# Kernel tuning notes

Measured on AMD Instinct MI355X. Metric: run time of the kernel, lower is better.

Reference implementation:

```python
import jax, jax.numpy as jnp
import numpy as np

B, T, K, V, D, C = 16, 16, 4, 10003, 256, 64  # batch, traj_len, beam, lid_size+3, dim_embed_loc, dim_com


def setup_inputs() -> dict:
    key = jax.random.key(0)
    ks = jax.random.split(key, 9)
    return {
        "loc_tar": jax.random.randint(ks[0], (B, T), 0, V),
        "zs": jax.random.normal(ks[1], (B, D), jnp.float32),
        "zt": jax.random.normal(ks[2], (B, D), jnp.float32),
        "E": jax.random.normal(ks[3], (V, D), jnp.float32) * 0.02,    # loc embedding table
        "W_v": jax.random.normal(ks[4], (D, V), jnp.float32) * 0.02,  # decoder output proj
        "b_v": jnp.zeros((V,), jnp.float32),
        "W_c": jax.random.normal(ks[5], (D, C), jnp.float32) * 0.05,  # LocCompressor
        "b_c": jnp.zeros((C,), jnp.float32),
        "W_t": jax.random.normal(ks[6], (C,), jnp.float32) * 0.05,    # temporal decoder
        "W_zt": jax.random.normal(ks[7], (D,), jnp.float32) * 0.05,
    }


def _decode(loc_tar, zs, E, W_v, b_v):
    # Beam-search decode faithful to the torch inference branch:
    # per-step full-seq decoder fwd, log_softmax, topk, (log-prob) product,
    # descending sort over M*K candidates, gather top 2K chains.
    chain_r = loc_tar.at[:, 1:].set(0)   # [B,T]; keep BOS, zero rest
    zs_r = zs                            # [B,D]
    prob = None
    for i in range(T - 1):
        emb = E[chain_r]                                     # [N,T,D] gather
        h = emb + zs_r[:, None, :]
        logp = jax.nn.log_softmax(h @ W_v + b_v, axis=-1)    # [N,T,V]
        p_i, idx_i = jax.lax.top_k(logp[:, i, :], K)         # [N,K]
        if i == 0:
            chain_r = jnp.repeat(chain_r, K, axis=0).at[:, 1].set(idx_i.reshape(-1))  # [B*K,T]
            prob = p_i                                       # [B,K]
            zs_r = jnp.repeat(zs_r, K, axis=0)
        else:
            M = chain_r.shape[0] // B                        # K at i=1, 2K after
            # NOTE: original multiplies log-probs (faithful to source)
            prob2 = (prob[:, :, None] * p_i.reshape(B, M, K)).reshape(B, M * K)
            order = jnp.argsort(-prob2, axis=-1)             # descending sort
            prob = jnp.take_along_axis(prob2, order, axis=-1)[:, :2 * K]
            ch = jnp.repeat(chain_r, K, axis=0).at[:, i + 1].set(idx_i.reshape(-1))
            ch = ch.reshape(B, M * K, T)
            chain_r = ch[jnp.arange(B)[:, None], order[:, :2 * K]].reshape(-1, T)  # [B*2K,T]
            zs_r = jnp.repeat(zs, 2 * K, axis=0)
    return chain_r.reshape(B, -1, T)[:, 0, 1:-1]             # best beam, [B,T-2]


def reference(loc_tar, zs, zt, E, W_v, b_v, W_c, b_c, W_t, W_zt):
    loc_chain = _decode(loc_tar, zs, E, W_v, b_v)            # [B,T-2] int
    loc_info = jnp.tanh(E[loc_chain] @ W_c + b_c)            # LocCompressor, [B,T-2,C]
    tim_chain = loc_info @ W_t + (zt @ W_zt)[:, None]        # temporal decoder, [B,T-2]
    return loc_chain, tim_chain
```

## Files before the change

### kernel.cpp

```cpp
#include <hip/hip_runtime.h>
#include <math.h>

#define BB 16
#define TT 16
#define KK 4
#define VV 10003
#define DD 256
#define CC 64
#define RPB 4
#define VT  1280
#define NVT 8
#define VP 10016
#define FNEG (-1e30f)

typedef float f32x4 __attribute__((ext_vector_type(4)));
typedef float f32x4u __attribute__((ext_vector_type(4), aligned(4)));

struct L4 { float v0, v1, v2, v3; int i0, i1, i2, i3; };

__device__ __forceinline__ void l4_init(L4 &l) {
  l.v0 = l.v1 = l.v2 = l.v3 = FNEG;
  l.i0 = l.i1 = l.i2 = l.i3 = 0x7fffffff;
}
__device__ __forceinline__ bool better(float v, int ix, float v2, int ix2) {
  return (v > v2) || (v == v2 && ix < ix2);
}
__device__ __forceinline__ void l4_insert(L4 &l, float v, int ix) {
  const bool c0 = better(v, ix, l.v0, l.i0);
  const bool c1 = better(v, ix, l.v1, l.i1);
  const bool c2 = better(v, ix, l.v2, l.i2);
  const bool c3 = better(v, ix, l.v3, l.i3);
  l.v3 = c3 ? (c2 ? l.v2 : v) : l.v3;  l.i3 = c3 ? (c2 ? l.i2 : ix) : l.i3;
  l.v2 = c2 ? (c1 ? l.v1 : v) : l.v2;  l.i2 = c2 ? (c1 ? l.i1 : ix) : l.i2;
  l.v1 = c1 ? (c0 ? l.v0 : v) : l.v1;  l.i1 = c1 ? (c0 ? l.i0 : ix) : l.i1;
  l.v0 = c0 ? v : l.v0;                l.i0 = c0 ? ix : l.i0;
}
__device__ __forceinline__ void l4_merge(L4 &a, const L4 &b) {
  l4_insert(a, b.v0, b.i0);
  l4_insert(a, b.v1, b.i1);
  l4_insert(a, b.v2, b.i2);
  l4_insert(a, b.v3, b.i3);
}
__device__ __forceinline__ L4 l4_shfl_xor(const L4 &a, int off) {
  L4 o;
  o.v0 = __shfl_xor(a.v0, off); o.i0 = __shfl_xor(a.i0, off);
  o.v1 = __shfl_xor(a.v1, off); o.i1 = __shfl_xor(a.i1, off);
  o.v2 = __shfl_xor(a.v2, off); o.i2 = __shfl_xor(a.i2, off);
  o.v3 = __shfl_xor(a.v3, off); o.i3 = __shfl_xor(a.i3, off);
  return o;
}

__device__ float np_block_sum(const float* a, int n) {
  float r0=a[0],r1=a[1],r2=a[2],r3=a[3],r4=a[4],r5=a[5],r6=a[6],r7=a[7];
  int i;
  for (i = 8; i + 8 <= n; i += 8) {
    r0 += a[i+0]; r1 += a[i+1]; r2 += a[i+2]; r3 += a[i+3];
    r4 += a[i+4]; r5 += a[i+5]; r6 += a[i+6]; r7 += a[i+7];
  }
  float res = ((r0 + r1) + (r2 + r3)) + ((r4 + r5) + (r6 + r7));
  for (; i < n; ++i) res += a[i];
  return res;
}

__global__ void k_init(const int* __restrict__ loc_tar, int* __restrict__ chainA) {
  int t = threadIdx.x;
  int b = t >> 4, j = t & 15;
  chainA[t] = (j == 0) ? loc_tar[b * TT] : 0;
}

__global__ __launch_bounds__(256, 1)
void k_gemm(const float* __restrict__ E, const float* __restrict__ zs,
            const float* __restrict__ Wv, const float* __restrict__ bv,
            const int* __restrict__ chain, float* __restrict__ Lg,
            int step, int N, int Mshift) {
  __shared__ __align__(16) float xs[RPB * DD];
  __shared__ int cs[RPB];

  const int t = threadIdx.x;
  const int tile = blockIdx.x % NVT;
  const int n0 = (blockIdx.x / NVT) * RPB;
  const int v0 = tile * VT;

  const int v4 = v0 + (t << 2);
  const int v1 = v0 + 1024 + t;
  const int v1ok = (v1 < VV);
  const int v1c = v1ok ? v1 : (VV - 1);

  if (t < RPB) {
    int n = n0 + t;
    int c = chain[n * TT + step];
    if ((unsigned)c >= VV) c = 0;
    cs[t] = c;
  }
  __syncthreads();

  for (int e = t; e < RPB * DD; e += 256) {
    int r = e >> 8, d = e & 255;
    int n = n0 + r;
    int b = n >> Mshift;
    xs[e] = E[cs[r] * DD + d] + zs[b * DD + d];
  }
  __syncthreads();

  const float* w4p = Wv + v4;
  const float* w1p = Wv + v1c;

  float acc4[RPB][4];
  float acc1[RPB];
#pragma unroll
  for (int r = 0; r < RPB; ++r) {
    acc1[r] = 0.f;
#pragma unroll
    for (int j = 0; j < 4; ++j) acc4[r][j] = 0.f;
  }

  f32x4u w4A[8], w4B[8];
  float  w1A[8], w1B[8];
  f32x4  h0A[RPB], h1A[RPB], h0B[RPB], h1B[RPB];

#pragma unroll
  for (int u = 0; u < 8; ++u) {
    w4A[u] = *(const f32x4u*)(w4p + (size_t)u * VV);
    w1A[u] = w1p[(size_t)u * VV];
  }
#pragma unroll
  for (int r = 0; r < RPB; ++r) {
    h0A[r] = *(const f32x4*)(xs + r * DD);
    h1A[r] = *(const f32x4*)(xs + r * DD + 4);
  }

  for (int d0 = 0; d0 < DD; d0 += 16) {
    const int dB = d0 + 8;
#pragma unroll
    for (int u = 0; u < 8; ++u) {
      w4B[u] = *(const f32x4u*)(w4p + (size_t)(dB + u) * VV);
      w1B[u] = w1p[(size_t)(dB + u) * VV];
    }
#pragma unroll
    for (int r = 0; r < RPB; ++r) {
      h0B[r] = *(const f32x4*)(xs + r * DD + dB);
      h1B[r] = *(const f32x4*)(xs + r * DD + dB + 4);
    }

#pragma unroll
    for (int u = 0; u < 8; ++u) {
#pragma unroll
      for (int r = 0; r < RPB; ++r) {
        const float hv = (u < 4) ? h0A[r][u] : h1A[r][u - 4];
#pragma unroll
        for (int j = 0; j < 4; ++j) acc4[r][j] = fmaf(hv, w4A[u][j], acc4[r][j]);
        acc1[r] = fmaf(hv, w1A[u], acc1[r]);
      }
    }

    const int dA = (d0 + 16 < DD) ? (d0 + 16) : 0;
#pragma unroll
    for (int u = 0; u < 8; ++u) {
      w4A[u] = *(const f32x4u*)(w4p + (size_t)(dA + u) * VV);
      w1A[u] = w1p[(size_t)(dA + u) * VV];
    }
#pragma unroll
    for (int r = 0; r < RPB; ++r) {
      h0A[r] = *(const f32x4*)(xs + r * DD + dA);
      h1A[r] = *(const f32x4*)(xs + r * DD + dA + 4);
    }

#pragma unroll
    for (int u = 0; u < 8; ++u) {
#pragma unroll
      for (int r = 0; r < RPB; ++r) {
        const float hv = (u < 4) ? h0B[r][u] : h1B[r][u - 4];
#pragma unroll
        for (int j = 0; j < 4; ++j) acc4[r][j] = fmaf(hv, w4B[u][j], acc4[r][j]);
        acc1[r] = fmaf(hv, w1B[u], acc1[r]);
      }
    }
  }

  const f32x4u bv4 = *(const f32x4u*)(bv + v4);
#pragma unroll
  for (int r = 0; r < RPB; ++r) {
    f32x4 o;
#pragma unroll
    for (int j = 0; j < 4; ++j) o[j] = acc4[r][j] + bv4[j];
    *(f32x4*)(Lg + (size_t)(n0 + r) * VP + v4) = o;
  }
  if (v1ok) {
    const float bvv = bv[v1];
#pragma unroll
    for (int r = 0; r < RPB; ++r)
      Lg[(size_t)(n0 + r) * VP + v1] = acc1[r] + bvv;
  }
}

__global__ __launch_bounds__(1024)
void k_red(const float* __restrict__ Lg, float* __restrict__ topP,
           int* __restrict__ topI) {
  __shared__ __align__(16) float row[VV];
  __shared__ float wmax[16];
  __shared__ float wv4[16 * 4];
  __shared__ int   wi4[16 * 4];

  const int n = blockIdx.x;
  const int t = threadIdx.x;
  const int lane = t & 63;
  const int wid = t >> 6;
  const float* grow = Lg + (size_t)n * VP;

  const int va = t << 2;
  const int vb = 4096 + (t << 2);
  const int vc = 8192 + (t << 2);
  f32x4 xa = *(const f32x4*)(grow + va);
  f32x4 xb = *(const f32x4*)(grow + vb);
  f32x4 xc;
  const bool cfull = (vc + 3 < VV);
  if (cfull) {
    xc = *(const f32x4*)(grow + vc);
  } else {
#pragma unroll
    for (int j = 0; j < 4; ++j) xc[j] = (vc + j < VV) ? grow[vc + j] : FNEG;
  }

  float m = FNEG;
  L4 top; l4_init(top);
#pragma unroll
  for (int j = 0; j < 4; ++j) { float x = xa[j]; if (x > m) m = x; l4_insert(top, x, va + j); }
#pragma unroll
  for (int j = 0; j < 4; ++j) { float x = xb[j]; if (x > m) m = x; l4_insert(top, x, vb + j); }
#pragma unroll
  for (int j = 0; j < 4; ++j) {
    if (vc + j < VV) { float x = xc[j]; if (x > m) m = x; l4_insert(top, x, vc + j); }
  }

  for (int off = 32; off; off >>= 1) {
    float m2 = __shfl_xor(m, off);
    if (m2 > m) m = m2;
    L4 o = l4_shfl_xor(top, off);
    l4_merge(top, o);
  }
  if (lane == 0) {
    wmax[wid] = m;
    wv4[wid * 4 + 0] = top.v0; wi4[wid * 4 + 0] = top.i0;
    wv4[wid * 4 + 1] = top.v1; wi4[wid * 4 + 1] = top.i1;
    wv4[wid * 4 + 2] = top.v2; wi4[wid * 4 + 2] = top.i2;
    wv4[wid * 4 + 3] = top.v3; wi4[wid * 4 + 3] = top.i3;
  }
  __syncthreads();

  float mm = wmax[lane & 15];
#pragma unroll
  for (int off = 8; off; off >>= 1) {
    float m2 = __shfl_xor(mm, off);
    if (m2 > mm) mm = m2;
  }
  const float gm = mm;

  L4 aa; l4_init(aa);
  if (wid == 0) {
    const int g = lane & 15;
    aa.v0 = wv4[g * 4 + 0]; aa.i0 = wi4[g * 4 + 0];
    aa.v1 = wv4[g * 4 + 1]; aa.i1 = wi4[g * 4 + 1];
    aa.v2 = wv4[g * 4 + 2]; aa.i2 = wi4[g * 4 + 2];
    aa.v3 = wv4[g * 4 + 3]; aa.i3 = wi4[g * 4 + 3];
#pragma unroll
    for (int off = 8; off; off >>= 1) {
      L4 o = l4_shfl_xor(aa, off);
      l4_merge(aa, o);
    }
  }

  {
    f32x4 ea, eb;
#pragma unroll
    for (int j = 0; j < 4; ++j) ea[j] = (float)exp((double)(xa[j] - gm));
#pragma unroll
    for (int j = 0; j < 4; ++j) eb[j] = (float)exp((double)(xb[j] - gm));
    *(f32x4*)(row + va) = ea;
    *(f32x4*)(row + vb) = eb;
    if (cfull) {
      f32x4 ec;
#pragma unroll
      for (int j = 0; j < 4; ++j) ec[j] = (float)exp((double)(xc[j] - gm));
      *(f32x4*)(row + vc) = ec;
    } else {
#pragma unroll
      for (int j = 0; j < 4; ++j)
        if (vc + j < VV) row[vc + j] = (float)exp((double)(xc[j] - gm));
    }
  }
  __syncthreads();

  if (t < 64) {
    int base = 0, nn = VV;
#pragma unroll
    for (int k = 5; k >= 0; --k) {
      int half = nn >> 1;
      int n2 = half - (half & 7);
      if ((t >> k) & 1) { base += n2; nn -= n2; } else nn = n2;
    }
    int half = nn >> 1;
    int n2 = half - (half & 7);
    float sa = np_block_sum(&row[base], n2);
    float sb = np_block_sum(&row[base + n2], nn - n2);
    float v = sa + sb;
#pragma unroll
    for (int l = 0; l < 6; ++l) {
      float x0 = __shfl(v, t * 2);
      float x1 = __shfl(v, t * 2 + 1);
      v = x0 + x1;
    }
    if (t == 0) {
      float ls = (float)log((double)v);
      topP[n * 4 + 0] = (aa.v0 - gm) - ls;  topI[n * 4 + 0] = aa.i0;
      topP[n * 4 + 1] = (aa.v1 - gm) - ls;  topI[n * 4 + 1] = aa.i1;
      topP[n * 4 + 2] = (aa.v2 - gm) - ls;  topI[n * 4 + 2] = aa.i2;
      topP[n * 4 + 3] = (aa.v3 - gm) - ls;  topI[n * 4 + 3] = aa.i3;
    }
  }
}

__global__ __launch_bounds__(512)
void k_beam(const float* __restrict__ topP, const int* __restrict__ topI,
            float* __restrict__ prob, const int* __restrict__ chain_cur,
            int* __restrict__ chain_next, int step) {
  __shared__ int sel_src[BB][8];
  __shared__ int sel_tok[BB][8];

  const int tid = threadIdx.x;
  const int b = tid >> 5;
  const int c = tid & 31;

  if (step == 0) {
    for (int e = tid; e < BB * KK * TT; e += 512) {
      int dst = e >> 4, q = e & 15;
      int bb = dst >> 2, kk = dst & 3;
      int val;
      if (q == 1) {
        int tok = topI[bb * 4 + kk]; if ((unsigned)tok >= VV) tok = 0;
        val = tok;
      } else {
        val = chain_cur[bb * TT + q];
      }
      chain_next[dst * TT + q] = val;
    }
    if (tid < BB * KK) {
      int bb = tid >> 2, kk = tid & 3;
      prob[bb * 8 + kk] = topP[bb * 4 + kk];
    }
    return;
  }

  const int M = (step == 1) ? 4 : 8;
  const int nc = M * 4;

  float act;
  if (c < nc) {
    int m = c >> 2, k = c & 3;
    act = prob[b * 8 + m] * topP[(b * M + m) * 4 + k];
  } else {
    act = -INFINITY;
  }

  for (int j = 0; j < 8; ++j) {
    float rv = act; int ri = c;
#pragma unroll
    for (int off = 1; off < 32; off <<= 1) {
      float v2 = __shfl_xor(rv, off, 32);
      int   i2 = __shfl_xor(ri, off, 32);
      if (v2 > rv || (v2 == rv && i2 < ri)) { rv = v2; ri = i2; }
    }
    if (c == ri) act = -INFINITY;
    if (c == 0) {
      int m = ri >> 2, k = ri & 3;
      int src = b * M + m;
      int tok = topI[src * 4 + k]; if ((unsigned)tok >= VV) tok = 0;
      sel_src[b][j] = src;
      sel_tok[b][j] = tok;
      prob[b * 8 + j] = rv;
    }
  }
  __syncthreads();

  for (int e = tid; e < BB * 8 * TT; e += 512) {
    int dst = e >> 4, q = e & 15;
    int bb = dst >> 3, j = dst & 7;
    int src = sel_src[bb][j];
    int val = (q == step + 1) ? sel_tok[bb][j] : chain_cur[src * TT + q];
    chain_next[dst * TT + q] = val;
  }
}

__global__ __launch_bounds__(64)
void k_final(const int* __restrict__ chain, const float* __restrict__ E,
             const float* __restrict__ Wc, const float* __restrict__ bc,
             const float* __restrict__ Wt, const float* __restrict__ zt,
             const float* __restrict__ Wzt, float* __restrict__ out) {
  int blk = blockIdx.x;
  int b = blk / (TT - 2), t = blk % (TT - 2);
  int lane = threadIdx.x;
  int loc = chain[(b * 8) * TT + 1 + t];
  if ((unsigned)loc >= VV) loc = 0;
  double acc = (double)bc[lane];
  const float* er = E + loc * DD;
  for (int d = 0; d < DD; ++d) acc += (double)er[d] * (double)Wc[d * CC + lane];
  double val = tanh(acc) * (double)Wt[lane];
  const float* ztr = zt + b * DD;
#pragma unroll
  for (int q = 0; q < 4; ++q) val += (double)ztr[lane * 4 + q] * (double)Wzt[lane * 4 + q];
  for (int off = 32; off; off >>= 1) val += __shfl_down(val, off);
  if (lane == 0) {
    out[b * (TT - 2) + t] = (float)loc;
    out[BB * (TT - 2) + b * (TT - 2) + t] = (float)val;
  }
}

extern "C" void kernel_launch(void* const* d_in, const int* in_sizes, int n_in,
                              void* d_out, int out_size, void* d_ws, size_t ws_size,
                              hipStream_t stream) {
  const int*   loc_tar = (const int*)  d_in[0];
  const float* zs      = (const float*)d_in[1];
  const float* zt      = (const float*)d_in[2];
  const float* E       = (const float*)d_in[3];
  const float* Wv      = (const float*)d_in[4];
  const float* bv      = (const float*)d_in[5];
  const float* Wc      = (const float*)d_in[6];
  const float* bc      = (const float*)d_in[7];
  const float* Wt      = (const float*)d_in[8];
  const float* Wzt     = (const float*)d_in[9];
  float* out = (float*)d_out;

  char* w = (char*)d_ws;
  float* Lg     = (float*)(w);
  float* topP   = (float*)(w + 5128192);
  int*   topI   = (int*)  (w + 5130240);
  float* prob   = (float*)(w + 5132288);
  int*   chainA = (int*)  (w + 5132800);
  int*   chainB = (int*)  (w + 5140992);

  k_init<<<1, 256, 0, stream>>>(loc_tar, chainA);

  int N = BB;
  int* cur = chainA;
  int* nxt = chainB;
  for (int i = 0; i < TT - 1; ++i) {
    int Mshift = (i == 0) ? 0 : ((i == 1) ? 2 : 3);
    int nrg = N / RPB;
    k_gemm<<<nrg * NVT, 256, 0, stream>>>(E, zs, Wv, bv, cur, Lg, i, N, Mshift);
    k_red<<<N, 1024, 0, stream>>>(Lg, topP, topI);
    k_beam<<<1, 512, 0, stream>>>(topP, topI, prob, cur, nxt, i);
    int* t2 = cur; cur = nxt; nxt = t2;
    N = (i == 0) ? BB * KK : BB * 2 * KK;
  }

  k_final<<<BB * (TT - 2), 64, 0, stream>>>(cur, E, Wc, bc, Wt, zt, Wzt, out);
}
```

Before: 1.017 ms.

## Fold beam selection into GEMM prologue and parallelize softmax sum

Drops the separate k_init and k_beam launches. Each k_gemm block now recomputes the beam top-2K selection redundantly in its prologue to get its input tokens, and block 0 writes the updated chain and prob buffers, which are double-buffered. k_final does the last selection itself. The softmax denominator in k_red now uses all 1024 threads (128 leaves, 8 lanes each, shuffle-reduced) instead of 64 serial leaves. This saves launch gaps and the serial sum, at the cost of redundant per-block selection work and a changed summation order.

```diff
diff --git a/kernel.cpp b/kernel.cpp
--- a/kernel.cpp
+++ b/kernel.cpp
@@ -50,31 +50,19 @@
   return o;
 }
 
-__device__ float np_block_sum(const float* a, int n) {
-  float r0=a[0],r1=a[1],r2=a[2],r3=a[3],r4=a[4],r5=a[5],r6=a[6],r7=a[7];
-  int i;
-  for (i = 8; i + 8 <= n; i += 8) {
-    r0 += a[i+0]; r1 += a[i+1]; r2 += a[i+2]; r3 += a[i+3];
-    r4 += a[i+4]; r5 += a[i+5]; r6 += a[i+6]; r7 += a[i+7];
-  }
-  float res = ((r0 + r1) + (r2 + r3)) + ((r4 + r5) + (r6 + r7));
-  for (; i < n; ++i) res += a[i];
-  return res;
-}
-
-__global__ void k_init(const int* __restrict__ loc_tar, int* __restrict__ chainA) {
-  int t = threadIdx.x;
-  int b = t >> 4, j = t & 15;
-  chainA[t] = (j == 0) ? loc_tar[b * TT] : 0;
-}
-
 __global__ __launch_bounds__(256, 1)
 void k_gemm(const float* __restrict__ E, const float* __restrict__ zs,
             const float* __restrict__ Wv, const float* __restrict__ bv,
-            const int* __restrict__ chain, float* __restrict__ Lg,
-            int step, int N, int Mshift) {
+            const int* __restrict__ loc_tar,
+            const float* __restrict__ topP, const int* __restrict__ topI,
+            const float* __restrict__ probIn, const int* __restrict__ chainIn,
+            float* __restrict__ probOut, int* __restrict__ chainOut,
+            float* __restrict__ Lg, int step, int N, int Mshift) {
   __shared__ __align__(16) float xs[RPB * DD];
   __shared__ int cs[RPB];
+  __shared__ int selSrc[BB][8];
+  __shared__ int selTok[BB][8];
+  __shared__ float prS[BB * 8];
 
   const int t = threadIdx.x;
   const int tile = blockIdx.x % NVT;
@@ -86,13 +74,79 @@
   const int v1ok = (v1 < VV);
   const int v1c = v1ok ? v1 : (VV - 1);
 
+  if (step >= 2) {
+    const int M = (step == 2) ? 4 : 8;
+    const int nc = M * 4;
+    const int c = t & 31;
+    const int bh = t >> 5;
+    for (int h = 0; h < 2; ++h) {
+      const int b = bh + h * 8;
+      float act;
+      if (c < nc) {
+        int mi = c >> 2, k = c & 3;
+        act = probIn[b * 8 + mi] * topP[(b * M + mi) * 4 + k];
+      } else {
+        act = -INFINITY;
+      }
+      for (int j = 0; j < 8; ++j) {
+        float rv = act; int ri = c;
+#pragma unroll
+        for (int off = 1; off < 32; off <<= 1) {
+          float v2 = __shfl_xor(rv, off, 32);
+          int   i2 = __shfl_xor(ri, off, 32);
+          if (v2 > rv || (v2 == rv && i2 < ri)) { rv = v2; ri = i2; }
+        }
+        if (c == ri) act = -INFINITY;
+        if (c == 0) {
+          int mi = ri >> 2, k = ri & 3;
+          int src = b * M + mi;
+          int tok = topI[src * 4 + k]; if ((unsigned)tok >= VV) tok = 0;
+          selSrc[b][j] = src;
+          selTok[b][j] = tok;
+          prS[b * 8 + j] = rv;
+        }
+      }
+    }
+    __syncthreads();
+  }
+
   if (t < RPB) {
     int n = n0 + t;
-    int c = chain[n * TT + step];
-    if ((unsigned)c >= VV) c = 0;
-    cs[t] = c;
+    int ctok;
+    if (step == 0)      ctok = loc_tar[n * TT];
+    else if (step == 1) ctok = topI[(n >> 2) * 4 + (n & 3)];
+    else                ctok = selTok[n >> 3][n & 7];
+    if ((unsigned)ctok >= VV) ctok = 0;
+    cs[t] = ctok;
   }
   __syncthreads();
+
+  if (blockIdx.x == 0 && step >= 1) {
+    if (step == 1) {
+      for (int e = t; e < BB * KK * TT; e += 256) {
+        int dst = e >> 4, q = e & 15;
+        int bb = dst >> 2, kk = dst & 3;
+        int val;
+        if (q == 1) { int tok = topI[bb * 4 + kk]; if ((unsigned)tok >= VV) tok = 0; val = tok; }
+        else if (q == 0) val = loc_tar[bb * TT];
+        else val = 0;
+        chainOut[dst * TT + q] = val;
+      }
+      if (t < BB * KK) {
+        int bb = t >> 2, kk = t & 3;
+        probOut[bb * 8 + kk] = topP[bb * 4 + kk];
+      }
+    } else {
+      for (int e = t; e < BB * 8 * TT; e += 256) {
+        int dst = e >> 4, q = e & 15;
+        int bb = dst >> 3, j = dst & 7;
+        int src = selSrc[bb][j];
+        int val = (q == step) ? selTok[bb][j] : chainIn[src * TT + q];
+        chainOut[dst * TT + q] = val;
+      }
+      if (t < BB * 8) probOut[t] = prS[t];
+    }
+  }
 
   for (int e = t; e < RPB * DD; e += 256) {
     int r = e >> 8, d = e & 255;
@@ -200,6 +254,7 @@
   __shared__ float wmax[16];
   __shared__ float wv4[16 * 4];
   __shared__ int   wi4[16 * 4];
+  __shared__ float leafS[128];
 
   const int n = blockIdx.x;
   const int t = threadIdx.x;
@@ -290,19 +345,31 @@
   }
   __syncthreads();
 
-  if (t < 64) {
+  {
+    const int g = t >> 3, j = t & 7;
     int base = 0, nn = VV;
 #pragma unroll
-    for (int k = 5; k >= 0; --k) {
+    for (int k = 6; k >= 0; --k) {
       int half = nn >> 1;
       int n2 = half - (half & 7);
-      if ((t >> k) & 1) { base += n2; nn -= n2; } else nn = n2;
-    }
-    int half = nn >> 1;
-    int n2 = half - (half & 7);
-    float sa = np_block_sum(&row[base], n2);
-    float sb = np_block_sum(&row[base + n2], nn - n2);
-    float v = sa + sb;
+      if ((g >> k) & 1) { base += n2; nn -= n2; } else nn = n2;
+    }
+    const float* a = row + base;
+    const int full = nn & ~7;
+    float r = a[j];
+    for (int i = 8 + j; i < full; i += 8) r += a[i];
+    float s = r + __shfl_xor(r, 1);
+    s = s + __shfl_xor(s, 2);
+    s = s + __shfl_xor(s, 4);
+    if (j == 0) {
+      for (int i = full; i < nn; ++i) s += a[i];
+      leafS[g] = s;
+    }
+  }
+  __syncthreads();
+
+  if (t < 64) {
+    float v = leafS[2 * t] + leafS[2 * t + 1];
 #pragma unroll
     for (int l = 0; l < 6; ++l) {
       float x0 = __shfl(v, t * 2);
@@ -319,87 +386,31 @@
   }
 }
 
-__global__ __launch_bounds__(512)
-void k_beam(const float* __restrict__ topP, const int* __restrict__ topI,
-            float* __restrict__ prob, const int* __restrict__ chain_cur,
-            int* __restrict__ chain_next, int step) {
-  __shared__ int sel_src[BB][8];
-  __shared__ int sel_tok[BB][8];
-
-  const int tid = threadIdx.x;
-  const int b = tid >> 5;
-  const int c = tid & 31;
-
-  if (step == 0) {
-    for (int e = tid; e < BB * KK * TT; e += 512) {
-      int dst = e >> 4, q = e & 15;
-      int bb = dst >> 2, kk = dst & 3;
-      int val;
-      if (q == 1) {
-        int tok = topI[bb * 4 + kk]; if ((unsigned)tok >= VV) tok = 0;
-        val = tok;
-      } else {
-        val = chain_cur[bb * TT + q];
-      }
-      chain_next[dst * TT + q] = val;
-    }
-    if (tid < BB * KK) {
-      int bb = tid >> 2, kk = tid & 3;
-      prob[bb * 8 + kk] = topP[bb * 4 + kk];
-    }
-    return;
-  }
-
-  const int M = (step == 1) ? 4 : 8;
-  const int nc = M * 4;
-
-  float act;
-  if (c < nc) {
-    int m = c >> 2, k = c & 3;
-    act = prob[b * 8 + m] * topP[(b * M + m) * 4 + k];
-  } else {
-    act = -INFINITY;
-  }
-
-  for (int j = 0; j < 8; ++j) {
-    float rv = act; int ri = c;
-#pragma unroll
-    for (int off = 1; off < 32; off <<= 1) {
-      float v2 = __shfl_xor(rv, off, 32);
-      int   i2 = __shfl_xor(ri, off, 32);
-      if (v2 > rv || (v2 == rv && i2 < ri)) { rv = v2; ri = i2; }
-    }
-    if (c == ri) act = -INFINITY;
-    if (c == 0) {
-      int m = ri >> 2, k = ri & 3;
-      int src = b * M + m;
-      int tok = topI[src * 4 + k]; if ((unsigned)tok >= VV) tok = 0;
-      sel_src[b][j] = src;
-      sel_tok[b][j] = tok;
-      prob[b * 8 + j] = rv;
-    }
-  }
-  __syncthreads();
-
-  for (int e = tid; e < BB * 8 * TT; e += 512) {
-    int dst = e >> 4, q = e & 15;
-    int bb = dst >> 3, j = dst & 7;
-    int src = sel_src[bb][j];
-    int val = (q == step + 1) ? sel_tok[bb][j] : chain_cur[src * TT + q];
-    chain_next[dst * TT + q] = val;
-  }
-}
-
 __global__ __launch_bounds__(64)
-void k_final(const int* __restrict__ chain, const float* __restrict__ E,
+void k_final(const int* __restrict__ chainIn, const float* __restrict__ probIn,
+             const float* __restrict__ topP, const int* __restrict__ topI,
+             const float* __restrict__ E,
              const float* __restrict__ Wc, const float* __restrict__ bc,
              const float* __restrict__ Wt, const float* __restrict__ zt,
              const float* __restrict__ Wzt, float* __restrict__ out) {
   int blk = blockIdx.x;
-  int b = blk / (TT - 2), t = blk % (TT - 2);
+  int b = blk / (TT - 2), tpos = blk % (TT - 2);
   int lane = threadIdx.x;
-  int loc = chain[(b * 8) * TT + 1 + t];
+
+  const int c = lane & 31;
+  int mi = c >> 2, k = c & 3;
+  float act = probIn[b * 8 + mi] * topP[(b * 8 + mi) * 4 + k];
+  float rv = act; int ri = c;
+#pragma unroll
+  for (int off = 1; off < 32; off <<= 1) {
+    float v2 = __shfl_xor(rv, off, 32);
+    int   i2 = __shfl_xor(ri, off, 32);
+    if (v2 > rv || (v2 == rv && i2 < ri)) { rv = v2; ri = i2; }
+  }
+  const int src = b * 8 + (ri >> 2);
+  int loc = chainIn[src * TT + 1 + tpos];
   if ((unsigned)loc >= VV) loc = 0;
+
   double acc = (double)bc[lane];
   const float* er = E + loc * DD;
   for (int d = 0; d < DD; ++d) acc += (double)er[d] * (double)Wc[d * CC + lane];
@@ -409,8 +420,8 @@
   for (int q = 0; q < 4; ++q) val += (double)ztr[lane * 4 + q] * (double)Wzt[lane * 4 + q];
   for (int off = 32; off; off >>= 1) val += __shfl_down(val, off);
   if (lane == 0) {
-    out[b * (TT - 2) + t] = (float)loc;
-    out[BB * (TT - 2) + b * (TT - 2) + t] = (float)val;
+    out[b * (TT - 2) + tpos] = (float)loc;
+    out[BB * (TT - 2) + b * (TT - 2) + tpos] = (float)val;
   }
 }
 
@@ -433,24 +444,28 @@
   float* Lg     = (float*)(w);
   float* topP   = (float*)(w + 5128192);
   int*   topI   = (int*)  (w + 5130240);
-  float* prob   = (float*)(w + 5132288);
-  int*   chainA = (int*)  (w + 5132800);
-  int*   chainB = (int*)  (w + 5140992);
-
-  k_init<<<1, 256, 0, stream>>>(loc_tar, chainA);
-
-  int N = BB;
-  int* cur = chainA;
-  int* nxt = chainB;
-  for (int i = 0; i < TT - 1; ++i) {
-    int Mshift = (i == 0) ? 0 : ((i == 1) ? 2 : 3);
-    int nrg = N / RPB;
-    k_gemm<<<nrg * NVT, 256, 0, stream>>>(E, zs, Wv, bv, cur, Lg, i, N, Mshift);
+  float* probA  = (float*)(w + 5132288);
+  float* probB  = (float*)(w + 5132800);
+  int*   chainA = (int*)  (w + 5133312);
+  int*   chainB = (int*)  (w + 5141504);
+
+  float* pIn = probA; float* pOut = probB;
+  int*   cIn = chainA; int*  cOut = chainB;
+
+  k_gemm<<<(16 / RPB) * NVT, 256, 0, stream>>>(E, zs, Wv, bv, loc_tar,
+      topP, topI, pIn, cIn, pOut, cOut, Lg, 0, 16, 0);
+  k_red<<<16, 1024, 0, stream>>>(Lg, topP, topI);
+
+  for (int i = 1; i < TT - 1; ++i) {
+    int N = (i == 1) ? (BB * KK) : (BB * 2 * KK);
+    int Mshift = (i == 1) ? 2 : 3;
+    k_gemm<<<(N / RPB) * NVT, 256, 0, stream>>>(E, zs, Wv, bv, loc_tar,
+        topP, topI, pIn, cIn, pOut, cOut, Lg, i, N, Mshift);
     k_red<<<N, 1024, 0, stream>>>(Lg, topP, topI);
-    k_beam<<<1, 512, 0, stream>>>(topP, topI, prob, cur, nxt, i);
-    int* t2 = cur; cur = nxt; nxt = t2;
-    N = (i == 0) ? BB * KK : BB * 2 * KK;
-  }
-
-  k_final<<<BB * (TT - 2), 64, 0, stream>>>(cur, E, Wc, bc, Wt, zt, Wzt, out);
-}
+    float* pt = pIn; pIn = pOut; pOut = pt;
+    int*   ct = cIn; cIn = cOut; cOut = ct;
+  }
+
+  k_final<<<BB * (TT - 2), 64, 0, stream>>>(cIn, pIn, topP, topI,
+                                            E, Wc, bc, Wt, zt, Wzt, out);
+}
```

Measured after the change: 1.019 ms. About the same (+0.2%).
